# Kernel optimization log

Hardware: AMD Instinct MI355X
Metric: run time of the kernel (lower is better)

Reference implementation:

```python
import jax, jax.numpy as jnp
import numpy as np

Q = 10        # icosahedral diamonds
M = 128       # 2**dggrid_level
L = Q * M * M # 163840 icosahedral points
KS = 9        # kernel_size / knn neighbors


def setup_inputs() -> dict:
    key = jax.random.key(0)
    k1, k2, k3, k4 = jax.random.split(key, 4)
    b, c, h, w = 1, 128, 256, 512
    x = jax.random.normal(k1, (b, c, h, w), dtype=jnp.float32)
    codeskmin = jax.random.randint(k2, (L, KS), 0, h * w, dtype=jnp.int32)
    att_w = jax.random.normal(k3, (KS, 2, KS), dtype=jnp.float32) * 0.1
    att_b = jnp.zeros((KS,), dtype=jnp.float32)
    depth_w = jax.random.normal(k4, (c, KS), dtype=jnp.float32) * 0.1
    depth_b = jnp.zeros((c,), dtype=jnp.float32)
    gamma = jnp.ones((c,), dtype=jnp.float32)
    beta = jnp.zeros((c,), dtype=jnp.float32)
    return {"x": x, "codeskmin": codeskmin, "att_w": att_w, "att_b": att_b,
            "depth_w": depth_w, "depth_b": depth_b, "gamma": gamma, "beta": beta}


def reference(x, codeskmin, att_w, att_b, depth_w, depth_b, gamma, beta):
    b, c, h, w = x.shape
    xf = x.reshape(b, c, h * w)
    # KNN gather: (b, c, L, KS)
    xe = xf[:, :, codeskmin]
    # --- SpatialAttentionModule_v1 ---
    avg = jnp.mean(xe, axis=1)           # (b, L, KS)
    mx = jnp.max(xe, axis=1)             # (b, L, KS)
    feat = jnp.stack([avg, mx], axis=1)  # (b, 2, L, KS)
    # Conv2d(2 -> KS, kernel (1,KS), no pad): reduces neighbor axis fully
    att = jnp.einsum('bilk,oik->bol', feat, att_w) + att_b[None, :, None]  # (b, KS, L)
    att = jax.nn.sigmoid(att)
    att = att.transpose(0, 2, 1)[:, None, :, :]  # (b, 1, L, KS)
    xe = att * xe + xe
    # --- depthwise conv over neighbor axis ---
    out = jnp.einsum('bclk,ck->bcl', xe, depth_w) + depth_b[None, :, None]  # (b, c, L)
    # rearrange 'b c (q h w) -> (b q) c h w'
    out = out.reshape(b, c, Q, M, M).transpose(0, 2, 1, 3, 4).reshape(b * Q, c, M, M)
    # BatchNorm (training-mode batch stats)
    mean = jnp.mean(out, axis=(0, 2, 3), keepdims=True)
    var = jnp.var(out, axis=(0, 2, 3), keepdims=True)
    out = (out - mean) * jax.lax.rsqrt(var + 1e-5)
    out = out * gamma[None, :, None, None] + beta[None, :, None, None]
    # Swish
    out = out * jax.nn.sigmoid(out)
    return out
```

## Files before the change

### kernel.cpp

```cpp
#include <hip/hip_runtime.h>
#include <hip/hip_bf16.h>

#define HW 131072
#define NCH 128
#define KS 9
#define L_TOTAL 163840
#define LPW 16

static __device__ __forceinline__ float bflo(unsigned int p) { return __uint_as_float(p << 16); }
static __device__ __forceinline__ float bfhi(unsigned int p) { return __uint_as_float(p & 0xffff0000u); }
static __device__ __forceinline__ unsigned short f2bf(float f) {
    unsigned int x = __float_as_uint(f);
    return (unsigned short)((x + 0x7fffu + ((x >> 16) & 1u)) >> 16);
}

__global__ __launch_bounds__(256) void transpose_x_kernel(
    const float2* __restrict__ xf,
    unsigned int* __restrict__ xT,
    float2* __restrict__ meanmaxP)
{
    __shared__ unsigned short tile[128 * 128];
    __shared__ float ps[4][128];
    __shared__ float pm[4][128];
    const int tid = threadIdx.x;
    const int lane = tid & 63;
    const int wave = tid >> 6;
    const int p0 = blockIdx.x * 128;
    const int pa = 2 * lane, pb = 2 * lane + 1;

    float s0 = 0.f, s1 = 0.f;
    float m0 = -3.4e38f, m1 = -3.4e38f;
    #pragma unroll 8
    for (int it = 0; it < 32; ++it) {
        int c = wave + (it << 2);
        float2 v = xf[(long)c * (HW / 2) + (p0 >> 1) + lane];
        tile[pa * 128 + ((c + 2 * pa) & 127)] = f2bf(v.x);
        tile[pb * 128 + ((c + 2 * pb) & 127)] = f2bf(v.y);
        s0 += v.x; s1 += v.y;
        m0 = fmaxf(m0, v.x); m1 = fmaxf(m1, v.y);
    }
    ps[wave][pa] = s0; ps[wave][pb] = s1;
    pm[wave][pa] = m0; pm[wave][pb] = m1;
    __syncthreads();

    #pragma unroll 8
    for (int it = 0; it < 32; ++it) {
        int p = wave + (it << 2);
        int colr = (2 * lane + 2 * p) & 127;
        unsigned int d = *reinterpret_cast<const unsigned int*>(&tile[p * 128 + colr]);
        xT[(long)(p0 + p) * 64 + lane] = d;
    }
    if (tid < 128) {
        float s = ps[0][tid] + ps[1][tid] + ps[2][tid] + ps[3][tid];
        float m = fmaxf(fmaxf(pm[0][tid], pm[1][tid]), fmaxf(pm[2][tid], pm[3][tid]));
        meanmaxP[p0 + tid] = make_float2(s * 0.0078125f, m);
    }
}

__global__ __launch_bounds__(256, 4) void encoder_main_kernel(
    const unsigned int* __restrict__ xT,
    const float2* __restrict__ meanmaxP,
    const int* __restrict__ cks,
    const float* __restrict__ att_w,
    const float* __restrict__ att_b,
    const float* __restrict__ depth_w,
    const float* __restrict__ depth_b,
    float* __restrict__ out,
    float* __restrict__ gsum, float* __restrict__ gsq)
{
    __shared__ __align__(16) char smem[38400];
    float* attw = (float*)smem;
    float* attb = (float*)(smem + 648);
    int*   lcks = (int*)(smem + 688);
    float* mult = (float*)(smem + 2992);
    float* tile = (float*)(smem + 5312);
    float* red  = (float*)smem;

    const int tid = threadIdx.x;
    const int lane = tid & 63;
    const int wave = tid >> 6;
    const int c0 = lane * 2, c1 = c0 + 1;
    const int base_l = blockIdx.x * 64;

    if (tid < 162) attw[tid] = att_w[tid];
    if (tid < KS) attb[tid] = att_b[tid];
    for (int j = tid; j < 64 * KS; j += 256) lcks[j] = cks[base_l * KS + j];

    float dw0[KS], dw1[KS];
    #pragma unroll
    for (int k = 0; k < KS; ++k) {
        dw0[k] = depth_w[c0 * KS + k];
        dw1[k] = depth_w[c1 * KS + k];
    }
    const float db0 = depth_b[c0], db1 = depth_b[c1];
    __syncthreads();

    {
        const int l_local = tid >> 2;
        const int sub = tid & 3;
        if (sub < 3) {
            float mean[KS], mx[KS];
            #pragma unroll
            for (int k = 0; k < KS; ++k) {
                float2 mm = meanmaxP[lcks[l_local * KS + k]];
                mean[k] = mm.x; mx[k] = mm.y;
            }
            #pragma unroll
            for (int oo = 0; oo < 3; ++oo) {
                int o = sub * 3 + oo;
                float logit = attb[o];
                #pragma unroll
                for (int k = 0; k < KS; ++k) {
                    logit = fmaf(mean[k], attw[o * 18 + k], logit);
                    logit = fmaf(mx[k],   attw[o * 18 + 9 + k], logit);
                }
                mult[l_local * KS + o] = 1.0f + 1.0f / (1.0f + __expf(-logit));
            }
        }
    }
    __syncthreads();

    float sum0 = 0.f, sum1 = 0.f, sq0 = 0.f, sq1 = 0.f;
    const int l0 = wave * LPW;

    unsigned int pv[KS], pn[KS];
    #pragma unroll
    for (int k = 0; k < KS; ++k) {
        int idx = __builtin_amdgcn_readfirstlane(lcks[l0 * KS + k]);
        pv[k] = xT[(long)idx * 64 + lane];
    }

    #pragma unroll
    for (int li = 0; li < LPW; ++li) {
        const int l_local = l0 + li;
        if (li + 1 < LPW) {
            #pragma unroll
            for (int k = 0; k < KS; ++k) {
                int idx = __builtin_amdgcn_readfirstlane(lcks[(l_local + 1) * KS + k]);
                pn[k] = xT[(long)idx * 64 + lane];
            }
        }
        float acc0 = db0, acc1 = db1;
        #pragma unroll
        for (int k = 0; k < KS; ++k) {
            float mk = mult[l_local * KS + k];
            acc0 = fmaf(bflo(pv[k]) * mk, dw0[k], acc0);
            acc1 = fmaf(bfhi(pv[k]) * mk, dw1[k], acc1);
        }
        tile[l_local * 129 + c0] = acc0;
        tile[l_local * 129 + c1] = acc1;
        sum0 += acc0; sum1 += acc1;
        sq0 = fmaf(acc0, acc0, sq0);
        sq1 = fmaf(acc1, acc1, sq1);
        #pragma unroll
        for (int k = 0; k < KS; ++k) pv[k] = pn[k];
    }

    __syncthreads();
    red[0 * 256 + tid] = sum0;
    red[1 * 256 + tid] = sum1;
    red[2 * 256 + tid] = sq0;
    red[3 * 256 + tid] = sq1;
    __syncthreads();

    const int q = base_l >> 14;
    const int r0 = base_l & 16383;
    #pragma unroll 8
    for (int it = 0; it < 32; ++it) {
        int c = wave + (it << 2);
        out[((long)(q * NCH + c) << 14) + r0 + lane] = tile[lane * 129 + c];
    }

    const int g = tid >> 6;
    const int i = tid & 63;
    float t = red[g * 256 + i] + red[g * 256 + 64 + i] +
              red[g * 256 + 128 + i] + red[g * 256 + 192 + i];
    float* dst = (g & 2) ? gsq : gsum;
    atomicAdd(&dst[2 * i + (g & 1)], t);
}

__global__ __launch_bounds__(256) void finalize_kernel(
    float4* __restrict__ out,
    const float* __restrict__ gsum, const float* __restrict__ gsq,
    const float* __restrict__ gamma, const float* __restrict__ beta)
{
    const long i4 = (long)blockIdx.x * 256 + threadIdx.x;
    const int c = (int)(i4 >> 12) & 127;

    const float invN = 1.0f / (float)L_TOTAL;
    const float m = gsum[c] * invN;
    const float var = gsq[c] * invN - m * m;
    const float sc = gamma[c] * rsqrtf(var + 1e-5f);
    const float sh = beta[c] - m * sc;

    float4 v = out[i4];
    float z0 = fmaf(v.x, sc, sh);
    float z1 = fmaf(v.y, sc, sh);
    float z2 = fmaf(v.z, sc, sh);
    float z3 = fmaf(v.w, sc, sh);
    v.x = z0 / (1.0f + __expf(-z0));
    v.y = z1 / (1.0f + __expf(-z1));
    v.z = z2 / (1.0f + __expf(-z2));
    v.w = z3 / (1.0f + __expf(-z3));
    out[i4] = v;
}

extern "C" void kernel_launch(void* const* d_in, const int* in_sizes, int n_in,
                              void* d_out, int out_size, void* d_ws, size_t ws_size,
                              hipStream_t stream) {
    const float2* x_f2 = (const float2*)d_in[0];
    const int* cks     = (const int*)d_in[1];
    const float* aw    = (const float*)d_in[2];
    const float* ab    = (const float*)d_in[3];
    const float* dw    = (const float*)d_in[4];
    const float* db    = (const float*)d_in[5];
    const float* gm    = (const float*)d_in[6];
    const float* bt    = (const float*)d_in[7];
    float* out         = (float*)d_out;

    char* ws = (char*)d_ws;
    unsigned int* xT  = (unsigned int*)ws;
    float2* meanmaxP  = (float2*)(ws + 33554432);
    float* gsum       = (float*)(ws + 33554432 + 1048576);
    float* gsq        = gsum + NCH;

    hipMemsetAsync(gsum, 0, 2 * NCH * sizeof(float), stream);

    transpose_x_kernel<<<HW / 128, 256, 0, stream>>>(x_f2, xT, meanmaxP);
    encoder_main_kernel<<<L_TOTAL / 64, 256, 0, stream>>>(
        xT, meanmaxP, cks, aw, ab, dw, db, out, gsum, gsq);
    finalize_kernel<<<out_size / 4 / 256, 256, 0, stream>>>(
        (float4*)out, gsum, gsq, gm, bt);
}
```

Baseline: 320.0 us.

## Store pre-norm activations as bf16 in workspace, add nontemporal loads/stores

The main kernel now packs its pre-BatchNorm outputs to bf16 and writes them to a workspace buffer instead of fp32 into the output. The finalize kernel reads that half-size buffer and writes fp32 to the output, which cuts intermediate write and read traffic. The smaller shared tile lets launch bounds rise from 4 to 7 blocks per SM, and nontemporal hints are added to streaming loads and stores. It adds bf16 rounding of intermediate values, which costs some accuracy.

After: 324.1 us. About the same (+1.3%).

```diff
diff --git a/kernel.cpp b/kernel.cpp
--- a/kernel.cpp
+++ b/kernel.cpp
@@ -7,15 +7,22 @@
 #define L_TOTAL 163840
 #define LPW 16
 
+typedef float        f32x2 __attribute__((ext_vector_type(2)));
+typedef float        f32x4 __attribute__((ext_vector_type(4)));
+typedef unsigned int u32x2 __attribute__((ext_vector_type(2)));
+
 static __device__ __forceinline__ float bflo(unsigned int p) { return __uint_as_float(p << 16); }
 static __device__ __forceinline__ float bfhi(unsigned int p) { return __uint_as_float(p & 0xffff0000u); }
 static __device__ __forceinline__ unsigned short f2bf(float f) {
     unsigned int x = __float_as_uint(f);
     return (unsigned short)((x + 0x7fffu + ((x >> 16) & 1u)) >> 16);
 }
+static __device__ __forceinline__ unsigned int pack2(float a, float b) {
+    return (unsigned int)f2bf(a) | ((unsigned int)f2bf(b) << 16);
+}
 
 __global__ __launch_bounds__(256) void transpose_x_kernel(
-    const float2* __restrict__ xf,
+    const f32x2* __restrict__ xf,
     unsigned int* __restrict__ xT,
     float2* __restrict__ meanmaxP)
 {
@@ -33,7 +40,7 @@
     #pragma unroll 8
     for (int it = 0; it < 32; ++it) {
         int c = wave + (it << 2);
-        float2 v = xf[(long)c * (HW / 2) + (p0 >> 1) + lane];
+        f32x2 v = __builtin_nontemporal_load(&xf[(long)c * (HW / 2) + (p0 >> 1) + lane]);
         tile[pa * 128 + ((c + 2 * pa) & 127)] = f2bf(v.x);
         tile[pb * 128 + ((c + 2 * pb) & 127)] = f2bf(v.y);
         s0 += v.x; s1 += v.y;
@@ -57,7 +64,7 @@
     }
 }
 
-__global__ __launch_bounds__(256, 4) void encoder_main_kernel(
+__global__ __launch_bounds__(256, 7) void encoder_main_kernel(
     const unsigned int* __restrict__ xT,
     const float2* __restrict__ meanmaxP,
     const int* __restrict__ cks,
@@ -65,15 +72,15 @@
     const float* __restrict__ att_b,
     const float* __restrict__ depth_w,
     const float* __restrict__ depth_b,
-    float* __restrict__ out,
+    unsigned int* __restrict__ ybuf,
     float* __restrict__ gsum, float* __restrict__ gsq)
 {
-    __shared__ __align__(16) char smem[38400];
+    __shared__ __align__(16) char smem[21952];
     float* attw = (float*)smem;
     float* attb = (float*)(smem + 648);
     int*   lcks = (int*)(smem + 688);
     float* mult = (float*)(smem + 2992);
-    float* tile = (float*)(smem + 5312);
+    unsigned int* tile = (unsigned int*)(smem + 5312);
     float* red  = (float*)smem;
 
     const int tid = threadIdx.x;
@@ -147,8 +154,7 @@
             acc0 = fmaf(bflo(pv[k]) * mk, dw0[k], acc0);
             acc1 = fmaf(bfhi(pv[k]) * mk, dw1[k], acc1);
         }
-        tile[l_local * 129 + c0] = acc0;
-        tile[l_local * 129 + c1] = acc1;
+        tile[l_local * 65 + lane] = pack2(acc0, acc1);
         sum0 += acc0; sum1 += acc1;
         sq0 = fmaf(acc0, acc0, sq0);
         sq1 = fmaf(acc1, acc1, sq1);
@@ -164,11 +170,18 @@
     __syncthreads();
 
     const int q = base_l >> 14;
-    const int r0 = base_l & 16383;
-    #pragma unroll 8
-    for (int it = 0; it < 32; ++it) {
-        int c = wave + (it << 2);
-        out[((long)(q * NCH + c) << 14) + r0 + lane] = tile[lane * 129 + c];
+    const int rp0 = (base_l & 16383) >> 1;
+    #pragma unroll
+    for (int it = 0; it < 16; ++it) {
+        int id = it * 256 + tid;
+        int c = id >> 5;
+        int rp = id & 31;
+        unsigned int t0 = tile[(2 * rp) * 65 + (c >> 1)];
+        unsigned int t1 = tile[(2 * rp + 1) * 65 + (c >> 1)];
+        unsigned short a = (c & 1) ? (unsigned short)(t0 >> 16) : (unsigned short)(t0 & 0xffff);
+        unsigned short b = (c & 1) ? (unsigned short)(t1 >> 16) : (unsigned short)(t1 & 0xffff);
+        unsigned int val = (unsigned int)a | ((unsigned int)b << 16);
+        __builtin_nontemporal_store(val, &ybuf[(long)(q * NCH + c) * 8192 + rp0 + rp]);
     }
 
     const int g = tid >> 6;
@@ -180,12 +193,13 @@
 }
 
 __global__ __launch_bounds__(256) void finalize_kernel(
-    float4* __restrict__ out,
+    const u32x2* __restrict__ ybuf,
     const float* __restrict__ gsum, const float* __restrict__ gsq,
-    const float* __restrict__ gamma, const float* __restrict__ beta)
+    const float* __restrict__ gamma, const float* __restrict__ beta,
+    f32x4* __restrict__ out)
 {
-    const long i4 = (long)blockIdx.x * 256 + threadIdx.x;
-    const int c = (int)(i4 >> 12) & 127;
+    const long j = (long)blockIdx.x * 256 + threadIdx.x;
+    const int c = (int)(j >> 12) & 127;
 
     const float invN = 1.0f / (float)L_TOTAL;
     const float m = gsum[c] * invN;
@@ -193,22 +207,23 @@
     const float sc = gamma[c] * rsqrtf(var + 1e-5f);
     const float sh = beta[c] - m * sc;
 
-    float4 v = out[i4];
-    float z0 = fmaf(v.x, sc, sh);
-    float z1 = fmaf(v.y, sc, sh);
-    float z2 = fmaf(v.z, sc, sh);
-    float z3 = fmaf(v.w, sc, sh);
+    u32x2 u = __builtin_nontemporal_load(&ybuf[j]);
+    float z0 = fmaf(bflo(u.x), sc, sh);
+    float z1 = fmaf(bfhi(u.x), sc, sh);
+    float z2 = fmaf(bflo(u.y), sc, sh);
+    float z3 = fmaf(bfhi(u.y), sc, sh);
+    f32x4 v;
     v.x = z0 / (1.0f + __expf(-z0));
     v.y = z1 / (1.0f + __expf(-z1));
     v.z = z2 / (1.0f + __expf(-z2));
     v.w = z3 / (1.0f + __expf(-z3));
-    out[i4] = v;
+    __builtin_nontemporal_store(v, &out[j]);
 }
 
 extern "C" void kernel_launch(void* const* d_in, const int* in_sizes, int n_in,
                               void* d_out, int out_size, void* d_ws, size_t ws_size,
                               hipStream_t stream) {
-    const float2* x_f2 = (const float2*)d_in[0];
+    const f32x2* x_f2  = (const f32x2*)d_in[0];
     const int* cks     = (const int*)d_in[1];
     const float* aw    = (const float*)d_in[2];
     const float* ab    = (const float*)d_in[3];
@@ -216,19 +231,19 @@
     const float* db    = (const float*)d_in[5];
     const float* gm    = (const float*)d_in[6];
     const float* bt    = (const float*)d_in[7];
-    float* out         = (float*)d_out;
 
     char* ws = (char*)d_ws;
-    unsigned int* xT  = (unsigned int*)ws;
-    float2* meanmaxP  = (float2*)(ws + 33554432);
-    float* gsum       = (float*)(ws + 33554432 + 1048576);
-    float* gsq        = gsum + NCH;
+    unsigned int* xT   = (unsigned int*)ws;
+    float2* meanmaxP   = (float2*)(ws + 33554432);
+    unsigned int* ybuf = (unsigned int*)(ws + 34603008);
+    float* gsum        = (float*)(ws + 34603008 + 41943040);
+    float* gsq         = gsum + NCH;
 
     hipMemsetAsync(gsum, 0, 2 * NCH * sizeof(float), stream);
 
     transpose_x_kernel<<<HW / 128, 256, 0, stream>>>(x_f2, xT, meanmaxP);
     encoder_main_kernel<<<L_TOTAL / 64, 256, 0, stream>>>(
-        xT, meanmaxP, cks, aw, ab, dw, db, out, gsum, gsq);
-    finalize_kernel<<<out_size / 4 / 256, 256, 0, stream>>>(
-        (float4*)out, gsum, gsq, gm, bt);
-}
+        xT, meanmaxP, cks, aw, ab, dw, db, ybuf, gsum, gsq);
+    finalize_kernel<<<20480, 256, 0, stream>>>(
+        (const u32x2*)ybuf, gsum, gsq, gm, bt, (f32x4*)d_out);
+}
```
